# Performance work log

Hardware: AMD Instinct MI355X
Metric: run time of the kernel (lower is better)

Reference implementation:

```python
import jax, jax.numpy as jnp
import numpy as np

EMBED_DIM = 1024
NUM_HEADS = 16
HEAD_DIM = EMBED_DIM // NUM_HEADS
B, T = 2, 2048


def setup_inputs() -> dict:
    key = jax.random.key(0)
    ks = jax.random.split(key, 10)
    s_in = 1.0 / np.sqrt(EMBED_DIM)
    s_hd = 1.0 / np.sqrt(HEAD_DIM)
    return {
        "hidden_states": jax.random.normal(ks[0], (B, T, EMBED_DIM), jnp.float32),
        "attn_mask": jnp.zeros((T, T), jnp.float32),
        # per-head parameter stacks (nn.Linear: y = x @ W^T + b); store W pre-transposed
        "W_q": jax.random.uniform(ks[1], (NUM_HEADS, EMBED_DIM, HEAD_DIM), jnp.float32, -s_in, s_in),
        "b_q": jax.random.uniform(ks[2], (NUM_HEADS, HEAD_DIM), jnp.float32, -s_in, s_in),
        "W_k": jax.random.uniform(ks[3], (NUM_HEADS, EMBED_DIM, HEAD_DIM), jnp.float32, -s_in, s_in),
        "b_k": jax.random.uniform(ks[4], (NUM_HEADS, HEAD_DIM), jnp.float32, -s_in, s_in),
        "W_v": jax.random.uniform(ks[5], (NUM_HEADS, EMBED_DIM, HEAD_DIM), jnp.float32, -s_in, s_in),
        "b_v": jax.random.uniform(ks[6], (NUM_HEADS, HEAD_DIM), jnp.float32, -s_in, s_in),
        "W_o": jax.random.uniform(ks[7], (NUM_HEADS, HEAD_DIM, EMBED_DIM), jnp.float32, -s_hd, s_hd),
        "b_o": jax.random.uniform(ks[8], (NUM_HEADS, EMBED_DIM), jnp.float32, -s_hd, s_hd),
        "gate": jnp.ones((NUM_HEADS,), jnp.float32),
    }


def reference(hidden_states, attn_mask, W_q, b_q, W_k, b_k, W_v, b_v, W_o, b_o, gate):
    # All heads: state='active', consent=True (defaults); dropout in eval mode.
    scale = 1.0 / np.sqrt(HEAD_DIM)
    # Q,K,V: [B,H,T,hd]
    Q = jnp.einsum("btd,hde->bhte", hidden_states, W_q) + b_q[None, :, None, :]
    K = jnp.einsum("btd,hde->bhte", hidden_states, W_k) + b_k[None, :, None, :]
    V = jnp.einsum("btd,hde->bhte", hidden_states, W_v) + b_v[None, :, None, :]
    scores = jnp.einsum("bhte,bhse->bhts", Q, K) * scale + attn_mask[None, None, :, :]
    weights = jax.nn.softmax(scores, axis=-1)
    out = jnp.einsum("bhts,bhse->bhte", weights, V)  # [B,H,T,hd]
    # per-head scalar norm: mean over (B,T) of L2 norm along head_dim, floored at 1e-5
    denom = jnp.maximum(
        jnp.sqrt(jnp.sum(out * out, axis=-1)).mean(axis=(0, 2)), 1e-5
    )  # [H]
    out_n = out / denom[None, :, None, None]
    g = jnp.clip(gate, 0.0, 1.0)  # gate_factor = 1.0 for 'active' heads
    # projected per head: (out_n @ W_o + b_o) * g; then sum over heads / H
    proj = (jnp.einsum("bhte,hed->bhtd", out_n, W_o) + b_o[None, :, None, :]) * g[None, :, None, None]
    return proj.sum(axis=1) / NUM_HEADS
```

## Files before the change

kernel.cpp:

```cpp
#include <hip/hip_runtime.h>
#include <hip/hip_bf16.h>
#include <math.h>

#define EMBED_DIM 1024
#define NUM_HEADS 16
#define HEAD_DIM  64
#define B_SZ      2
#define T_SZ      2048
#define BT        (B_SZ * T_SZ)
#define LOG2E     1.44269504088896340736f
#define QSCALE    (0.125f * LOG2E)
#define SOFT_OFF  8.0f

typedef short bf16x8 __attribute__((ext_vector_type(8)));
typedef float f32x4  __attribute__((ext_vector_type(4)));

#define MFMA16(a, b, c) __builtin_amdgcn_mfma_f32_16x16x32_bf16((a), (b), (c), 0, 0, 0)

__device__ inline short f2bf(float f) {
    unsigned u = __builtin_bit_cast(unsigned, f);
    u = (u + 0x7fffu + ((u >> 16) & 1u)) >> 16;
    return (short)u;
}
__device__ inline float bf2f(short s) {
    unsigned u = ((unsigned)(unsigned short)s) << 16;
    return __builtin_bit_cast(float, u);
}
__device__ inline unsigned pk2(float a, float b) {
#if __has_builtin(__builtin_amdgcn_cvt_pk_bf16_f32)
    typedef __bf16 bf2_t __attribute__((ext_vector_type(2)));
    bf2_t t = __builtin_amdgcn_cvt_pk_bf16_f32(a, b);
    return __builtin_bit_cast(unsigned, t);
#else
    return (unsigned)(unsigned short)f2bf(a) | ((unsigned)(unsigned short)f2bf(b) << 16);
#endif
}

__device__ inline void gld16(const short* g, short* lds) {
    __builtin_amdgcn_global_load_lds(
        (const __attribute__((address_space(1))) void*)g,
        (__attribute__((address_space(3))) void*)lds, 16, 0, 0);
}

__device__ inline bf16x8 frag_swz(const short* tile, int R, int C) {
    return *(const bf16x8*)(tile + R * 64 + ((C ^ (R & 7)) << 3));
}

__device__ inline float red_add64(float v) {
    v += __shfl_xor(v, 1); v += __shfl_xor(v, 2); v += __shfl_xor(v, 4);
    v += __shfl_xor(v, 8); v += __shfl_xor(v, 16); v += __shfl_xor(v, 32);
    return v;
}

__global__ __launch_bounds__(256) void cvt_in_kernel(
    const float* __restrict__ hs, short* __restrict__ hsb)
{
    const long i = ((long)blockIdx.x * 256 + threadIdx.x) * 4;
    const float4 v = *(const float4*)(hs + i);
    ushort4 o; o.x = f2bf(v.x); o.y = f2bf(v.y); o.z = f2bf(v.z); o.w = f2bf(v.w);
    *(ushort4*)(hsb + i) = o;
}

__global__ __launch_bounds__(256) void transpose_w_kernel(
    const float* __restrict__ Wq, const float* __restrict__ Wk,
    const float* __restrict__ Wv, const float* __restrict__ Wo,
    short* __restrict__ Wqt, short* __restrict__ Wkt,
    short* __restrict__ Wvt, short* __restrict__ WoT)
{
    const int arr = blockIdx.z, h = blockIdx.y;
    const float* src; short* dst; int R, C;
    if (arr == 0)      { src = Wq; dst = Wqt; R = 1024; C = 64; }
    else if (arr == 1) { src = Wk; dst = Wkt; R = 1024; C = 64; }
    else if (arr == 2) { src = Wv; dst = Wvt; R = 1024; C = 64; }
    else               { src = Wo; dst = WoT; R = 64;   C = 1024; }
    src += (long)h * 65536; dst += (long)h * 65536;

    const int ct = C / 32;
    const int tr = blockIdx.x / ct, tc = blockIdx.x % ct;
    __shared__ float tile[32][33];
    const int tx = threadIdx.x & 31, ty = threadIdx.x >> 5;
    #pragma unroll
    for (int i = 0; i < 4; ++i) {
        const int r = ty + 8 * i;
        tile[r][tx] = src[(long)(tr * 32 + r) * C + tc * 32 + tx];
    }
    __syncthreads();
    #pragma unroll
    for (int i = 0; i < 4; ++i) {
        const int r = ty + 8 * i;
        dst[(long)(tc * 32 + r) * R + tr * 32 + tx] = f2bf(tile[tx][r]);
    }
}

__global__ __launch_bounds__(256) void qkv_mfma_kernel(
    const short* __restrict__ hsb,
    const short* __restrict__ Wt,
    const float* __restrict__ bq, const float* __restrict__ bk,
    const float* __restrict__ bv,
    short* __restrict__ Qb, short* __restrict__ Kb, short* __restrict__ Vtb)
{
    const int m0 = blockIdx.x * 128;
    const int n0 = blockIdx.y * 128;
    __shared__ short As[128 * 64];
    __shared__ short Bs[128 * 64];

    const int tid = threadIdx.x, lane = tid & 63, w = tid >> 6;
    const int wm = w & 1, wn = w >> 1;
    const int quad = lane >> 4, l15 = lane & 15;

    f32x4 acc[4][4] = {};

    for (int k0 = 0; k0 < 1024; k0 += 64) {
        __syncthreads();
        #pragma unroll
        for (int t = 0; t < 4; ++t) {
            const int r0 = w * 32 + t * 8;
            const int r  = r0 + (lane >> 3);
            const int cg = (lane & 7) ^ (r & 7);
            gld16(hsb + (long)(m0 + r) * 1024 + k0 + cg * 8, &As[r0 * 64]);
            gld16(Wt  + (long)(n0 + r) * 1024 + k0 + cg * 8, &Bs[r0 * 64]);
        }
        __syncthreads();
        #pragma unroll
        for (int ks = 0; ks < 2; ++ks) {
            bf16x8 af[4];
            #pragma unroll
            for (int ms = 0; ms < 4; ++ms)
                af[ms] = frag_swz(As, wm * 64 + ms * 16 + l15, ks * 4 + quad);
            #pragma unroll
            for (int ns = 0; ns < 4; ++ns) {
                const bf16x8 bfr = frag_swz(Bs, wn * 64 + ns * 16 + l15, ks * 4 + quad);
                #pragma unroll
                for (int ms = 0; ms < 4; ++ms)
                    acc[ms][ns] = MFMA16(af[ms], bfr, acc[ms][ns]);
            }
        }
    }

    #pragma unroll
    for (int ns = 0; ns < 4; ++ns) {
        const int n    = n0 + wn * 64 + ns * 16 + l15;
        const int type = n >> 10;
        const int h    = (n >> 6) & 15;
        const int e    = n & 63;
        const float bias = (type == 0 ? bq : type == 1 ? bk : bv)[h * 64 + e];
        #pragma unroll
        for (int ms = 0; ms < 4; ++ms) {
            const int mbase = m0 + wm * 64 + ms * 16 + quad * 4;
            const int bb = mbase >> 11, t0 = mbase & 2047;
            if (type == 2) {
                const int tp = (t0 & ~63) | (t0 & 35) | ((t0 & 12) << 1) | ((t0 & 16) >> 2);
                ushort4 pk;
                pk.x = (unsigned short)f2bf(acc[ms][ns][0] + bias);
                pk.y = (unsigned short)f2bf(acc[ms][ns][1] + bias);
                pk.z = (unsigned short)f2bf(acc[ms][ns][2] + bias);
                pk.w = (unsigned short)f2bf(acc[ms][ns][3] + bias);
                *(ushort4*)&Vtb[((long)(bb * 16 + h) * 64 + e) * 2048 + tp] = pk;
            } else {
                #pragma unroll
                for (int r = 0; r < 4; ++r) {
                    const float v = acc[ms][ns][r] + bias;
                    const long off = ((long)(bb * 16 + h) * 2048 + (t0 + r)) * 64 + e;
                    if (type == 0) Qb[off] = f2bf(v * QSCALE);
                    else           Kb[off] = f2bf(v);
                }
            }
        }
    }
}

__global__ __launch_bounds__(256) void attn_mfma_kernel(
    const short* __restrict__ Qb, const short* __restrict__ Kb,
    const short* __restrict__ Vtb, const float* __restrict__ maskf,
    short* __restrict__ Ob, float* __restrict__ denomsum)
{
    const int q0 = blockIdx.x * 128;
    const int h  = blockIdx.y, b = blockIdx.z;
    const long bh = ((long)b * 16 + h) * (long)T_SZ * 64;

    __shared__ short Ks[64 * 64];
    __shared__ short Vs[64 * 64];
    __shared__ float wred[4];

    const int tid = threadIdx.x, lane = tid & 63, w = tid >> 6;
    const int quad = lane >> 4, l15 = lane & 15;
    const int qrowA = q0 + w * 32 + l15;

    const short* Kg = Kb + bh;
    const short* Vg = Vtb + bh;

    bf16x8 qf[2][2];
    #pragma unroll
    for (int qs = 0; qs < 2; ++qs)
        #pragma unroll
        for (int ks = 0; ks < 2; ++ks)
            qf[qs][ks] = *(const bf16x8*)(Qb + bh +
                (long)(qrowA + qs * 16) * 64 + ks * 32 + quad * 8);

    f32x4 o[2][4] = {};
    float lp[2] = {0.f, 0.f};

    const float* mrowA = maskf + (long)qrowA * 2048 + quad * 4;

    for (int kt = 0; kt < 32; ++kt) {
        const int kv0 = kt * 64;

        float4 mv[2][4];
        #pragma unroll
        for (int qs = 0; qs < 2; ++qs)
            #pragma unroll
            for (int kb = 0; kb < 4; ++kb)
                mv[qs][kb] = *(const float4*)(mrowA + (long)qs * 16 * 2048 + kv0 + kb * 16);

        __syncthreads();
        #pragma unroll
        for (int t = 0; t < 2; ++t) {
            const int r0 = w * 16 + t * 8;
            const int r  = r0 + (lane >> 3);
            const int cg = (lane & 7) ^ (r & 7);
            gld16(Kg + (long)(kv0 + r) * 64 + cg * 8, &Ks[r0 * 64]);
            gld16(Vg + (long)r * 2048 + kv0 + cg * 8, &Vs[r0 * 64]);
        }
        __syncthreads();

        #pragma unroll
        for (int qs = 0; qs < 2; ++qs) {
            f32x4 s[4];
            #pragma unroll
            for (int kb = 0; kb < 4; ++kb) {
                s[kb][0] = fmaf(mv[qs][kb].x, LOG2E, -SOFT_OFF);
                s[kb][1] = fmaf(mv[qs][kb].y, LOG2E, -SOFT_OFF);
                s[kb][2] = fmaf(mv[qs][kb].z, LOG2E, -SOFT_OFF);
                s[kb][3] = fmaf(mv[qs][kb].w, LOG2E, -SOFT_OFF);
            }
            #pragma unroll
            for (int ks = 0; ks < 2; ++ks)
                #pragma unroll
                for (int kb = 0; kb < 4; ++kb) {
                    const bf16x8 kf = frag_swz(Ks, kb * 16 + l15, ks * 4 + quad);
                    s[kb] = MFMA16(kf, qf[qs][ks], s[kb]);
                }

            float rs = 0.f;
            unsigned w0[4], w1[4];
            #pragma unroll
            for (int kb = 0; kb < 4; ++kb) {
                const float p0 = exp2f(s[kb][0]);
                const float p1 = exp2f(s[kb][1]);
                const float p2 = exp2f(s[kb][2]);
                const float p3 = exp2f(s[kb][3]);
                rs += (p0 + p1) + (p2 + p3);
                w0[kb] = pk2(p0, p1);
                w1[kb] = pk2(p2, p3);
            }
            lp[qs] += rs;

            #pragma unroll
            for (int kbp = 0; kbp < 2; ++kbp) {
                const uint4 u = {w0[2 * kbp], w1[2 * kbp], w0[2 * kbp + 1], w1[2 * kbp + 1]};
                const bf16x8 pb = __builtin_bit_cast(bf16x8, u);
                #pragma unroll
                for (int eb = 0; eb < 4; ++eb) {
                    const bf16x8 va = frag_swz(Vs, eb * 16 + l15, kbp * 4 + quad);
                    o[qs][eb] = MFMA16(va, pb, o[qs][eb]);
                }
            }
        }
    }

    float tot = 0.f;
    #pragma unroll
    for (int qs = 0; qs < 2; ++qs) {
        float lf = lp[qs];
        lf += __shfl_xor(lf, 16);
        lf += __shfl_xor(lf, 32);
        const float inv = 1.f / lf;
        float ss = 0.f;
        #pragma unroll
        for (int eb = 0; eb < 4; ++eb) {
            o[qs][eb] *= inv;
            #pragma unroll
            for (int r = 0; r < 4; ++r) ss += o[qs][eb][r] * o[qs][eb][r];
        }
        ss += __shfl_xor(ss, 16);
        ss += __shfl_xor(ss, 32);
        tot += sqrtf(ss);

        const int qrow = qrowA + qs * 16;
        #pragma unroll
        for (int eb = 0; eb < 4; ++eb) {
            uint2 pk;
            pk.x = pk2(o[qs][eb][0], o[qs][eb][1]);
            pk.y = pk2(o[qs][eb][2], o[qs][eb][3]);
            *(uint2*)&Ob[((long)(b * 2048 + qrow)) * 1024 + h * 64 + eb * 16 + quad * 4] = pk;
        }
    }
    const float wsum = red_add64(tot) * 0.25f;
    if (lane == 0) wred[w] = wsum;
    __syncthreads();
    if (tid == 0)
        atomicAdd(&denomsum[h], wred[0] + wred[1] + wred[2] + wred[3]);
}

__global__ __launch_bounds__(256) void scale_w_kernel(
    short* __restrict__ WoT, const float* __restrict__ denomsum,
    const float* __restrict__ gate)
{
    __shared__ float sh[16];
    if (threadIdx.x < 16) {
        const float g  = fminf(fmaxf(gate[threadIdx.x], 0.f), 1.f);
        const float dn = fmaxf(denomsum[threadIdx.x] * (1.f / (float)BT), 1e-5f);
        sh[threadIdx.x] = g / (dn * (float)NUM_HEADS);
    }
    __syncthreads();
    const long i = ((long)blockIdx.x * 256 + threadIdx.x) * 4;
    const float sc = sh[(int)(i >> 16)];
    ushort4 v = *(ushort4*)(WoT + i);
    v.x = (unsigned short)f2bf(bf2f((short)v.x) * sc);
    v.y = (unsigned short)f2bf(bf2f((short)v.y) * sc);
    v.z = (unsigned short)f2bf(bf2f((short)v.z) * sc);
    v.w = (unsigned short)f2bf(bf2f((short)v.w) * sc);
    *(ushort4*)(WoT + i) = v;
}

__global__ __launch_bounds__(256) void oproj_mfma_kernel(
    const short* __restrict__ Ob,
    const short* __restrict__ WoT,
    const float* __restrict__ bo,
    const float* __restrict__ gate,
    float* __restrict__ out)
{
    const int m0 = blockIdx.x * 128;
    const int n0 = blockIdx.y * 128;
    __shared__ short As[2][128 * 64];
    __shared__ short Bs[2][128 * 64];

    const int tid = threadIdx.x, lane = tid & 63, w = tid >> 6;
    const int wm = w & 1, wn = w >> 1;
    const int quad = lane >> 4, l15 = lane & 15;

    auto stage = [&](int h, int buf) {
        #pragma unroll
        for (int t = 0; t < 4; ++t) {
            const int r0 = w * 32 + t * 8;
            const int r  = r0 + (lane >> 3);
            const int cg = (lane & 7) ^ (r & 7);
            gld16(Ob + (long)(m0 + r) * 1024 + h * 64 + cg * 8, &As[buf][r0 * 64]);
            gld16(WoT + (long)h * 65536 + (long)(n0 + r) * 64 + cg * 8, &Bs[buf][r0 * 64]);
        }
    };

    f32x4 acc[4][4] = {};
    stage(0, 0);

    for (int h = 0; h < 16; ++h) {
        const int cur = h & 1;
        __syncthreads();
        if (h < 15) stage(h + 1, cur ^ 1);
        #pragma unroll
        for (int ks = 0; ks < 2; ++ks) {
            bf16x8 af[4];
            #pragma unroll
            for (int ms = 0; ms < 4; ++ms)
                af[ms] = frag_swz(&As[cur][0], wm * 64 + ms * 16 + l15, ks * 4 + quad);
            #pragma unroll
            for (int ns = 0; ns < 4; ++ns) {
                const bf16x8 bfr = frag_swz(&Bs[cur][0], wn * 64 + ns * 16 + l15, ks * 4 + quad);
                #pragma unroll
                for (int ms = 0; ms < 4; ++ms)
                    acc[ms][ns] = MFMA16(af[ms], bfr, acc[ms][ns]);
            }
        }
    }

    float gcl[16];
    #pragma unroll
    for (int hh = 0; hh < 16; ++hh)
        gcl[hh] = fminf(fmaxf(gate[hh], 0.f), 1.f) * (1.f / (float)NUM_HEADS);

    #pragma unroll
    for (int ns = 0; ns < 4; ++ns) {
        const int n = n0 + wn * 64 + ns * 16 + l15;
        float be = 0.f;
        #pragma unroll
        for (int hh = 0; hh < 16; ++hh) be += gcl[hh] * bo[hh * 1024 + n];
        #pragma unroll
        for (int ms = 0; ms < 4; ++ms) {
            const int m = m0 + wm * 64 + ms * 16 + quad * 4;
            #pragma unroll
            for (int r = 0; r < 4; ++r)
                out[(long)(m + r) * 1024 + n] = acc[ms][ns][r] + be;
        }
    }
}

extern "C" void kernel_launch(void* const* d_in, const int* in_sizes, int n_in,
                              void* d_out, int out_size, void* d_ws, size_t ws_size,
                              hipStream_t stream)
{
    const float* hs   = (const float*)d_in[0];
    const float* mask = (const float*)d_in[1];
    const float* Wq   = (const float*)d_in[2];
    const float* bq   = (const float*)d_in[3];
    const float* Wk   = (const float*)d_in[4];
    const float* bk   = (const float*)d_in[5];
    const float* Wv   = (const float*)d_in[6];
    const float* bv   = (const float*)d_in[7];
    const float* Wo   = (const float*)d_in[8];
    const float* bo   = (const float*)d_in[9];
    const float* gate = (const float*)d_in[10];
    float* out = (float*)d_out;

    char* ws = (char*)d_ws;
    const size_t MB = 1024 * 1024;
    short* hsb   = (short*)(ws);
    short* Wqt   = (short*)(ws + 8  * MB);
    short* Wkt   = (short*)(ws + 10 * MB);
    short* Wvt   = (short*)(ws + 12 * MB);
    short* WoT   = (short*)(ws + 14 * MB);
    short* Qb    = (short*)(ws + 16 * MB);
    short* Kb    = (short*)(ws + 24 * MB);
    short* Vtb   = (short*)(ws + 32 * MB);
    short* Ob    = (short*)(ws + 40 * MB);
    float* denomsum = (float*)(ws + 48 * MB);

    (void)hipMemsetAsync(denomsum, 0, NUM_HEADS * sizeof(float), stream);

    cvt_in_kernel<<<4096, 256, 0, stream>>>(hs, hsb);
    transpose_w_kernel<<<dim3(64, 16, 4), 256, 0, stream>>>(
        Wq, Wk, Wv, Wo, Wqt, Wkt, Wvt, WoT);
    qkv_mfma_kernel<<<dim3(32, 24), 256, 0, stream>>>(
        hsb, Wqt, bq, bk, bv, Qb, Kb, Vtb);
    attn_mfma_kernel<<<dim3(16, 16, 2), 256, 0, stream>>>(
        Qb, Kb, Vtb, mask, Ob, denomsum);
    scale_w_kernel<<<1024, 256, 0, stream>>>(WoT, denomsum, gate);
    oproj_mfma_kernel<<<dim3(32, 8), 256, 0, stream>>>(
        Ob, WoT, bo, gate, out);
}
```

Baseline: 260.6 us.

## Widen attention KV tile to 128, use hardware exp2, halve o-proj M tile

The attention kernel now stages 128 keys per iteration, with two 64-wide V sub-tiles, and processes them in an inner loop. This halves the number of barrier-synchronised load phases. exp2f is replaced with the amdgcn exp2 intrinsic to skip the range handling in the libm version. The output projection uses 64-row M tiles and launches twice as many blocks to improve occupancy and CU coverage on the small GEMM. The trade-offs are more LDS and registers per attention block, and more redundant W_o tile loads in the projection.

```diff
diff --git a/kernel.cpp b/kernel.cpp
--- a/kernel.cpp
+++ b/kernel.cpp
@@ -33,6 +33,13 @@
     return __builtin_bit_cast(unsigned, t);
 #else
     return (unsigned)(unsigned short)f2bf(a) | ((unsigned)(unsigned short)f2bf(b) << 16);
+#endif
+}
+__device__ inline float fast_exp2(float x) {
+#if __has_builtin(__builtin_amdgcn_exp2f)
+    return __builtin_amdgcn_exp2f(x);
+#else
+    return exp2f(x);
 #endif
 }
 
@@ -178,8 +185,8 @@
     const int h  = blockIdx.y, b = blockIdx.z;
     const long bh = ((long)b * 16 + h) * (long)T_SZ * 64;
 
-    __shared__ short Ks[64 * 64];
-    __shared__ short Vs[64 * 64];
+    __shared__ short Ks[128 * 64];
+    __shared__ short Vs[2][64 * 64];
     __shared__ float wred[4];
 
     const int tid = threadIdx.x, lane = tid & 63, w = tid >> 6;
@@ -202,67 +209,83 @@
 
     const float* mrowA = maskf + (long)qrowA * 2048 + quad * 4;
 
-    for (int kt = 0; kt < 32; ++kt) {
-        const int kv0 = kt * 64;
-
-        float4 mv[2][4];
+    for (int kt = 0; kt < 16; ++kt) {
+        const int kv0 = kt * 128;
+
+        float4 mv[2][2][4];
         #pragma unroll
         for (int qs = 0; qs < 2; ++qs)
             #pragma unroll
-            for (int kb = 0; kb < 4; ++kb)
-                mv[qs][kb] = *(const float4*)(mrowA + (long)qs * 16 * 2048 + kv0 + kb * 16);
+            for (int j = 0; j < 2; ++j)
+                #pragma unroll
+                for (int kb = 0; kb < 4; ++kb)
+                    mv[qs][j][kb] = *(const float4*)(mrowA +
+                        (long)qs * 16 * 2048 + kv0 + j * 64 + kb * 16);
 
         __syncthreads();
         #pragma unroll
-        for (int t = 0; t < 2; ++t) {
-            const int r0 = w * 16 + t * 8;
+        for (int t = 0; t < 4; ++t) {
+            const int r0 = w * 32 + t * 8;
             const int r  = r0 + (lane >> 3);
             const int cg = (lane & 7) ^ (r & 7);
             gld16(Kg + (long)(kv0 + r) * 64 + cg * 8, &Ks[r0 * 64]);
-            gld16(Vg + (long)r * 2048 + kv0 + cg * 8, &Vs[r0 * 64]);
-        }
+        }
+        #pragma unroll
+        for (int j = 0; j < 2; ++j)
+            #pragma unroll
+            for (int t = 0; t < 2; ++t) {
+                const int r0 = w * 16 + t * 8;
+                const int r  = r0 + (lane >> 3);
+                const int cg = (lane & 7) ^ (r & 7);
+                gld16(Vg + (long)r * 2048 + kv0 + j * 64 + cg * 8, &Vs[j][r0 * 64]);
+            }
         __syncthreads();
 
         #pragma unroll
-        for (int qs = 0; qs < 2; ++qs) {
-            f32x4 s[4];
-            #pragma unroll
-            for (int kb = 0; kb < 4; ++kb) {
-                s[kb][0] = fmaf(mv[qs][kb].x, LOG2E, -SOFT_OFF);
-                s[kb][1] = fmaf(mv[qs][kb].y, LOG2E, -SOFT_OFF);
-                s[kb][2] = fmaf(mv[qs][kb].z, LOG2E, -SOFT_OFF);
-                s[kb][3] = fmaf(mv[qs][kb].w, LOG2E, -SOFT_OFF);
-            }
-            #pragma unroll
-            for (int ks = 0; ks < 2; ++ks)
+        for (int j = 0; j < 2; ++j) {
+            const short* Ksub = Ks + j * 64 * 64;
+            #pragma unroll
+            for (int qs = 0; qs < 2; ++qs) {
+                f32x4 s[4];
                 #pragma unroll
                 for (int kb = 0; kb < 4; ++kb) {
-                    const bf16x8 kf = frag_swz(Ks, kb * 16 + l15, ks * 4 + quad);
-                    s[kb] = MFMA16(kf, qf[qs][ks], s[kb]);
+                    s[kb][0] = fmaf(mv[qs][j][kb].x, LOG2E, -SOFT_OFF);
+                    s[kb][1] = fmaf(mv[qs][j][kb].y, LOG2E, -SOFT_OFF);
+                    s[kb][2] = fmaf(mv[qs][j][kb].z, LOG2E, -SOFT_OFF);
+                    s[kb][3] = fmaf(mv[qs][j][kb].w, LOG2E, -SOFT_OFF);
                 }
-
-            float rs = 0.f;
-            unsigned w0[4], w1[4];
-            #pragma unroll
-            for (int kb = 0; kb < 4; ++kb) {
-                const float p0 = exp2f(s[kb][0]);
-                const float p1 = exp2f(s[kb][1]);
-                const float p2 = exp2f(s[kb][2]);
-                const float p3 = exp2f(s[kb][3]);
-                rs += (p0 + p1) + (p2 + p3);
-                w0[kb] = pk2(p0, p1);
-                w1[kb] = pk2(p2, p3);
-            }
-            lp[qs] += rs;
-
-            #pragma unroll
-            for (int kbp = 0; kbp < 2; ++kbp) {
-                const uint4 u = {w0[2 * kbp], w1[2 * kbp], w0[2 * kbp + 1], w1[2 * kbp + 1]};
-                const bf16x8 pb = __builtin_bit_cast(bf16x8, u);
-                #pragma unroll
-                for (int eb = 0; eb < 4; ++eb) {
-                    const bf16x8 va = frag_swz(Vs, eb * 16 + l15, kbp * 4 + quad);
-                    o[qs][eb] = MFMA16(va, pb, o[qs][eb]);
+                #pragma unroll
+                for (int ks = 0; ks < 2; ++ks)
+                    #pragma unroll
+                    for (int kb = 0; kb < 4; ++kb) {
+                        const bf16x8 kf = frag_swz(Ksub, kb * 16 + l15, ks * 4 + quad);
+                        s[kb] = MFMA16(kf, qf[qs][ks], s[kb]);
+                    }
+
+                float rs = 0.f;
+                unsigned w0[4], w1[4];
+                #pragma unroll
+                for (int kb = 0; kb < 4; ++kb) {
+                    const float p0 = fast_exp2(s[kb][0]);
+                    const float p1 = fast_exp2(s[kb][1]);
+                    const float p2 = fast_exp2(s[kb][2]);
+                    const float p3 = fast_exp2(s[kb][3]);
+                    rs += (p0 + p1) + (p2 + p3);
+                    w0[kb] = pk2(p0, p1);
+                    w1[kb] = pk2(p2, p3);
+                }
+                lp[qs] += rs;
+
+                #pragma unroll
+                for (int kbp = 0; kbp < 2; ++kbp) {
+                    const uint4 u = {w0[2 * kbp], w1[2 * kbp],
+                                     w0[2 * kbp + 1], w1[2 * kbp + 1]};
+                    const bf16x8 pb = __builtin_bit_cast(bf16x8, u);
+                    #pragma unroll
+                    for (int eb = 0; eb < 4; ++eb) {
+                        const bf16x8 va = frag_swz(&Vs[j][0], eb * 16 + l15, kbp * 4 + quad);
+                        o[qs][eb] = MFMA16(va, pb, o[qs][eb]);
+                    }
                 }
             }
         }
@@ -330,9 +353,9 @@
     const float* __restrict__ gate,
     float* __restrict__ out)
 {
-    const int m0 = blockIdx.x * 128;
+    const int m0 = blockIdx.x * 64;
     const int n0 = blockIdx.y * 128;
-    __shared__ short As[2][128 * 64];
+    __shared__ short As[2][64 * 64];
     __shared__ short Bs[2][128 * 64];
 
     const int tid = threadIdx.x, lane = tid & 63, w = tid >> 6;
@@ -340,17 +363,23 @@
     const int quad = lane >> 4, l15 = lane & 15;
 
     auto stage = [&](int h, int buf) {
+        #pragma unroll
+        for (int t = 0; t < 2; ++t) {
+            const int r0 = w * 16 + t * 8;
+            const int r  = r0 + (lane >> 3);
+            const int cg = (lane & 7) ^ (r & 7);
+            gld16(Ob + (long)(m0 + r) * 1024 + h * 64 + cg * 8, &As[buf][r0 * 64]);
+        }
         #pragma unroll
         for (int t = 0; t < 4; ++t) {
             const int r0 = w * 32 + t * 8;
             const int r  = r0 + (lane >> 3);
             const int cg = (lane & 7) ^ (r & 7);
-            gld16(Ob + (long)(m0 + r) * 1024 + h * 64 + cg * 8, &As[buf][r0 * 64]);
             gld16(WoT + (long)h * 65536 + (long)(n0 + r) * 64 + cg * 8, &Bs[buf][r0 * 64]);
         }
     };
 
-    f32x4 acc[4][4] = {};
+    f32x4 acc[2][4] = {};
     stage(0, 0);
 
     for (int h = 0; h < 16; ++h) {
@@ -359,15 +388,15 @@
         if (h < 15) stage(h + 1, cur ^ 1);
         #pragma unroll
         for (int ks = 0; ks < 2; ++ks) {
-            bf16x8 af[4];
-            #pragma unroll
-            for (int ms = 0; ms < 4; ++ms)
-                af[ms] = frag_swz(&As[cur][0], wm * 64 + ms * 16 + l15, ks * 4 + quad);
+            bf16x8 af[2];
+            #pragma unroll
+            for (int ms = 0; ms < 2; ++ms)
+                af[ms] = frag_swz(&As[cur][0], wm * 32 + ms * 16 + l15, ks * 4 + quad);
             #pragma unroll
             for (int ns = 0; ns < 4; ++ns) {
                 const bf16x8 bfr = frag_swz(&Bs[cur][0], wn * 64 + ns * 16 + l15, ks * 4 + quad);
                 #pragma unroll
-                for (int ms = 0; ms < 4; ++ms)
+                for (int ms = 0; ms < 2; ++ms)
                     acc[ms][ns] = MFMA16(af[ms], bfr, acc[ms][ns]);
             }
         }
@@ -385,8 +414,8 @@
         #pragma unroll
         for (int hh = 0; hh < 16; ++hh) be += gcl[hh] * bo[hh * 1024 + n];
         #pragma unroll
-        for (int ms = 0; ms < 4; ++ms) {
-            const int m = m0 + wm * 64 + ms * 16 + quad * 4;
+        for (int ms = 0; ms < 2; ++ms) {
+            const int m = m0 + wm * 32 + ms * 16 + quad * 4;
             #pragma unroll
             for (int r = 0; r < 4; ++r)
                 out[(long)(m + r) * 1024 + n] = acc[ms][ns][r] + be;
@@ -434,6 +463,6 @@
     attn_mfma_kernel<<<dim3(16, 16, 2), 256, 0, stream>>>(
         Qb, Kb, Vtb, mask, Ob, denomsum);
     scale_w_kernel<<<1024, 256, 0, stream>>>(WoT, denomsum, gate);
-    oproj_mfma_kernel<<<dim3(32, 8), 256, 0, stream>>>(
+    oproj_mfma_kernel<<<dim3(64, 8), 256, 0, stream>>>(
         Ob, WoT, bo, gate, out);
 }
```

After: 260.7 us. Within noise of the previous version (+0.0%).
